# Performance work log

Measured on AMD Instinct MI355X. Metric: run time of the kernel, lower is better.

## Reference

```python
import jax, jax.numpy as jnp
import numpy as np

B, IN_DIM, HIDDEN, N_CLASSES, D_Z = 16384, 1024, 2048, 8, 256
LN_EPS = 1e-5  # torch.nn.LayerNorm default


def _l2_normalize(x, axis=1, eps=1e-12):
    # matches F.normalize: x / max(||x||, eps)
    n = jnp.sqrt(jnp.sum(x * x, axis=axis, keepdims=True))
    return x / jnp.maximum(n, eps)


def setup_inputs() -> dict:
    key = jax.random.key(0)
    ks = jax.random.split(key, 9)
    s1 = 1.0 / np.sqrt(IN_DIM)
    s2 = 1.0 / np.sqrt(HIDDEN)
    return {
        "feat": jax.random.normal(ks[0], (B, IN_DIM), dtype=jnp.float32),
        "z_cat": jax.random.normal(ks[1], (B, D_Z), dtype=jnp.float32),
        "mu_cat": jax.random.normal(ks[2], (N_CLASSES, D_Z), dtype=jnp.float32),
        "ln_gamma": jnp.ones((N_CLASSES, IN_DIM), dtype=jnp.float32),
        "ln_beta": jnp.zeros((N_CLASSES, IN_DIM), dtype=jnp.float32),
        "W1": jax.random.uniform(ks[3], (N_CLASSES, IN_DIM, HIDDEN), jnp.float32, -s1, s1),
        "b1": jax.random.uniform(ks[4], (N_CLASSES, HIDDEN), jnp.float32, -s1, s1),
        "W2": jax.random.uniform(ks[5], (N_CLASSES, HIDDEN, N_CLASSES), jnp.float32, -s2, s2),
        "b2": jax.random.uniform(ks[6], (N_CLASSES, N_CLASSES), jnp.float32, -s2, s2),
        "tau_gate": 1,
    }


def reference(feat, z_cat, mu_cat, ln_gamma, ln_beta, W1, b1, W2, b2, tau_gate):
    # --- cosine-similarity softmax gate ---
    zn = _l2_normalize(z_cat, axis=1)            # [B, Dz]
    mun = _l2_normalize(mu_cat, axis=1)          # [E, Dz]
    sims = zn @ mun.T                            # [B, E]
    tau = max(1e-6, float(tau_gate))
    w = jax.nn.softmax(sims / tau, axis=1)       # [B, E]

    # --- batched experts: LN -> Linear -> ReLU -> (Dropout=identity, eval) -> Linear ---
    mu = jnp.mean(feat, axis=-1, keepdims=True)
    var = jnp.mean(jnp.square(feat - mu), axis=-1, keepdims=True)
    xhat = (feat - mu) * jax.lax.rsqrt(var + LN_EPS)            # [B, D] (shared)
    x_e = xhat[None] * ln_gamma[:, None, :] + ln_beta[:, None, :]  # [E, B, D]
    h = jax.nn.relu(jnp.einsum('ebd,edh->ebh', x_e, W1) + b1[:, None, :])  # [E, B, H]
    exp_logits = jnp.einsum('ebh,ehc->ebc', h, W2) + b2[:, None, :]        # [E, B, C]

    # --- gate-weighted sum over experts ---
    logits = jnp.einsum('ebc,be->bc', exp_logits, w)  # [B, C]
    return logits, w
```

## Files before the change

kernel.cpp:

```cpp
#include <hip/hip_runtime.h>
#include <hip/hip_bf16.h>
#include <cstdint>

#define NB     16384
#define DIN    1024
#define HID    2048
#define NE     8
#define NC     8
#define DZ     256

#define BK2    64
#define NKT    (DIN / BK2)
#define GRID_MAIN 256

typedef short bf16x8 __attribute__((ext_vector_type(8)));
typedef float f32x4  __attribute__((ext_vector_type(4)));

__device__ __forceinline__ unsigned short f2bf(float f) {
    unsigned int u = __float_as_uint(f);
    unsigned int r = (u + 0x7FFFu + ((u >> 16) & 1u)) >> 16;
    return (unsigned short)r;
}

__device__ __forceinline__ void async_copy16(const void* g, void* l) {
    __builtin_amdgcn_global_load_lds(
        (const __attribute__((address_space(1))) unsigned int*)g,
        (__attribute__((address_space(3))) unsigned int*)l, 16, 0, 0);
}

__global__ __launch_bounds__(256) void k_pre(const float* __restrict__ feat,
                                             unsigned short* __restrict__ xhat,
                                             const float* __restrict__ z,
                                             const float* __restrict__ mu,
                                             const int* __restrict__ tau_i,
                                             const float* __restrict__ b2,
                                             float* __restrict__ wout,
                                             float* __restrict__ logits) {
    if (blockIdx.x < NB) {
        int row = blockIdx.x;
        int t = threadIdx.x;
        float4 v = *(const float4*)&feat[(size_t)row * DIN + t * 4];
        float s  = v.x + v.y + v.z + v.w;
        float sq = v.x * v.x + v.y * v.y + v.z * v.z + v.w * v.w;
#pragma unroll
        for (int off = 32; off; off >>= 1) {
            s  += __shfl_down(s, off);
            sq += __shfl_down(sq, off);
        }
        __shared__ float ls[8];
        int w = t >> 6, l = t & 63;
        if (l == 0) { ls[w] = s; ls[4 + w] = sq; }
        __syncthreads();
        s  = ls[0] + ls[1] + ls[2] + ls[3];
        sq = ls[4] + ls[5] + ls[6] + ls[7];
        float mean = s * (1.f / DIN);
        float var  = sq * (1.f / DIN) - mean * mean;
        float r = 1.0f / sqrtf(var + 1e-5f);
        uint2 p;
        p.x = (unsigned)f2bf((v.x - mean) * r) | ((unsigned)f2bf((v.y - mean) * r) << 16);
        p.y = (unsigned)f2bf((v.z - mean) * r) | ((unsigned)f2bf((v.w - mean) * r) << 16);
        *(uint2*)&xhat[(size_t)row * DIN + t * 4] = p;
    } else {
        int row = (blockIdx.x - NB) * 4 + (threadIdx.x >> 6);
        int l = threadIdx.x & 63;
        float4 zv = *(const float4*)&z[(size_t)row * DZ + l * 4];
        float zz = zv.x * zv.x + zv.y * zv.y + zv.z * zv.z + zv.w * zv.w;
        float dots[NE], mm[NE];
#pragma unroll
        for (int e = 0; e < NE; ++e) {
            float4 m = *(const float4*)&mu[e * DZ + l * 4];
            dots[e] = zv.x * m.x + zv.y * m.y + zv.z * m.z + zv.w * m.w;
            mm[e]   = m.x * m.x + m.y * m.y + m.z * m.z + m.w * m.w;
        }
#pragma unroll
        for (int off = 32; off; off >>= 1) {
            zz += __shfl_xor(zz, off);
#pragma unroll
            for (int e = 0; e < NE; ++e) {
                dots[e] += __shfl_xor(dots[e], off);
                mm[e]   += __shfl_xor(mm[e], off);
            }
        }
        float zn = fmaxf(sqrtf(zz), 1e-12f);
        float tau = fmaxf(1e-6f, (float)tau_i[0]);
        float s[NE], mx = -1e30f;
#pragma unroll
        for (int e = 0; e < NE; ++e) {
            s[e] = dots[e] / (zn * fmaxf(sqrtf(mm[e]), 1e-12f)) / tau;
            mx = fmaxf(mx, s[e]);
        }
        float sum = 0.f;
#pragma unroll
        for (int e = 0; e < NE; ++e) { s[e] = expf(s[e] - mx); sum += s[e]; }
        float inv = 1.f / sum;
        if (l < NE) {
            wout[(size_t)row * NE + l] = s[l] * inv;
            float acc = 0.f;
#pragma unroll
            for (int e = 0; e < NE; ++e) acc += s[e] * inv * b2[e * NC + l];
            logits[(size_t)row * NC + l] = acc;
        }
    }
}

__global__ __launch_bounds__(256) void k_w2prep(const float* __restrict__ W2,
                                                const float* __restrict__ b1,
                                                unsigned short* __restrict__ w2t,
                                                float* __restrict__ b1p) {
    int i = blockIdx.x * 256 + threadIdx.x;
    int e = i >> 15;
    int rem = i & 32767;
    int c = rem >> 11;
    int h = rem & 2047;
    float v = (c < NC) ? W2[((size_t)(e * HID + h)) * NC + c] : 0.f;
    w2t[i] = f2bf(v);
    if (i < NE * HID) b1p[i] = b1[i];
}

__global__ __launch_bounds__(256) void k_w1prep(const float* __restrict__ W1,
                                                const float* __restrict__ gamma,
                                                const float* __restrict__ beta,
                                                unsigned short* __restrict__ w1t,
                                                float* __restrict__ b1p) {
    __shared__ float tile[64][65];
    int e  = blockIdx.z;
    int d0 = blockIdx.y * 64;
    int h0 = blockIdx.x * 64;
    int tx = threadIdx.x & 15, ty = threadIdx.x >> 4;
#pragma unroll
    for (int rr = 0; rr < 4; ++rr) {
        int d = ty + rr * 16;
        float4 v = *(const float4*)&W1[((size_t)e * DIN + d0 + d) * HID + h0 + tx * 4];
        tile[tx * 4 + 0][d] = v.x;
        tile[tx * 4 + 1][d] = v.y;
        tile[tx * 4 + 2][d] = v.z;
        tile[tx * 4 + 3][d] = v.w;
    }
    __syncthreads();
    float4 g = *(const float4*)&gamma[(size_t)e * DIN + d0 + tx * 4];
#pragma unroll
    for (int rr = 0; rr < 4; ++rr) {
        int h = ty + rr * 16;
        uint2 p;
        p.x = (unsigned)f2bf(tile[h][tx * 4 + 0] * g.x) |
              ((unsigned)f2bf(tile[h][tx * 4 + 1] * g.y) << 16);
        p.y = (unsigned)f2bf(tile[h][tx * 4 + 2] * g.z) |
              ((unsigned)f2bf(tile[h][tx * 4 + 3] * g.w) << 16);
        *(uint2*)&w1t[((size_t)e * HID + h0 + h) * DIN + d0 + tx * 4] = p;
    }
    if (threadIdx.x < 64) {
        int h = threadIdx.x;
        float sacc = 0.f;
        for (int r = 0; r < 64; ++r)
            sacc += beta[(size_t)e * DIN + d0 + r] * tile[h][r];
        atomicAdd(&b1p[(size_t)e * HID + h0 + h], sacc);
    }
}


#define WAITV(n_) asm volatile("s_waitcnt vmcnt(" #n_ ")" ::: "memory")
#define BAR()  do { __builtin_amdgcn_s_barrier(); __builtin_amdgcn_sched_barrier(0); } while (0)

#define STAGE(gAp_, gBp_, kt64_, par_) do {                                   \
    char* da_ = (char*)lds + ((par_) << 16) + (t << 4);                       \
    const size_t ko_ = sbase + (size_t)(kt64_) * BK2;                         \
    async_copy16((gAp_) + ko_,          da_);                                 \
    async_copy16((gAp_) + ko_ + 65536,  da_ + 8192);                          \
    async_copy16((gAp_) + ko_ + 131072, da_ + 16384);                         \
    async_copy16((gAp_) + ko_ + 196608, da_ + 24576);                         \
    async_copy16((gBp_) + ko_,          da_ + 32768);                         \
    async_copy16((gBp_) + ko_ + 65536,  da_ + 40960);                         \
    async_copy16((gBp_) + ko_ + 131072, da_ + 49152);                         \
    async_copy16((gBp_) + ko_ + 196608, da_ + 57344);                         \
} while (0)

#define KBODY(par_) do {                                                      \
    const short* la_ = (const short*)(lds + ((par_) << 16));                  \
    const short* lb_ = la_ + 16384;                                           \
    {                                                                         \
        bf16x8 bF_[4];                                                        \
        _Pragma("unroll")                                                     \
        for (int j_ = 0; j_ < 4; ++j_)                                        \
            bF_[j_] = *(const bf16x8*)&lb_[(wn + 16 * j_ + ml) * BK2 + csw0]; \
        __builtin_amdgcn_s_setprio(1);                                        \
        _Pragma("unroll")                                                     \
        for (int i_ = 0; i_ < 8; ++i_) {                                      \
            const bf16x8 aF_ =                                                \
                *(const bf16x8*)&la_[(wm + 16 * i_ + ml) * BK2 + csw0];       \
            _Pragma("unroll")                                                 \
            for (int j_ = 0; j_ < 4; ++j_)                                    \
                acc[i_][j_] = __builtin_amdgcn_mfma_f32_16x16x32_bf16(        \
                    aF_, bF_[j_], acc[i_][j_], 0, 0, 0);                      \
        }                                                                     \
        __builtin_amdgcn_s_setprio(0);                                        \
    }                                                                         \
    {                                                                         \
        const int cs1_ = csw0 ^ 32;                                           \
        bf16x8 bF_[4];                                                        \
        _Pragma("unroll")                                                     \
        for (int j_ = 0; j_ < 4; ++j_)                                        \
            bF_[j_] = *(const bf16x8*)&lb_[(wn + 16 * j_ + ml) * BK2 + cs1_]; \
        __builtin_amdgcn_s_setprio(1);                                        \
        _Pragma("unroll")                                                     \
        for (int i_ = 0; i_ < 8; ++i_) {                                      \
            const bf16x8 aF_ =                                                \
                *(const bf16x8*)&la_[(wm + 16 * i_ + ml) * BK2 + cs1_];       \
            _Pragma("unroll")                                                 \
            for (int j_ = 0; j_ < 4; ++j_)                                    \
                acc[i_][j_] = __builtin_amdgcn_mfma_f32_16x16x32_bf16(        \
                    aF_, bF_[j_], acc[i_][j_], 0, 0, 0);                      \
        }                                                                     \
        __builtin_amdgcn_s_setprio(0);                                        \
    }                                                                         \
} while (0)

__global__ __launch_bounds__(512, 2) void moe_main(
        const unsigned short* __restrict__ xhat,
        const unsigned short* __restrict__ w1t,
        const float* __restrict__ b1p,
        const unsigned short* __restrict__ w2t,
        const float* __restrict__ wg,
        float* __restrict__ logits) {
    __shared__ __align__(16) char lds[131072];

    const int t  = threadIdx.x;
    const int w  = t >> 6, l = t & 63;
    const int q  = l >> 4, ml = l & 15;
    const int wm = (w >> 2) * 128;
    const int wn = (w & 3) * 64;
    const int csw0 = (q ^ (ml & 7)) * 8;
    const size_t sbase = (size_t)(t >> 3) * DIN +
                         (size_t)(((t & 7) ^ ((t >> 3) & 7)) * 8);

    const int e    = blockIdx.x & 7;
    const int slot = blockIdx.x >> 3;
    char* myht = (char*)lds + 65536 + w * 5120;
    const unsigned short* eA = w1t + (size_t)e * HID * DIN;

    STAGE(eA, xhat + (size_t)slot * 256 * DIN, 0, 0);

    for (int pr = 0; pr < 2; ++pr) {
        const int b0 = (pr * 32 + slot) * 256;
        const unsigned short* gB = xhat + (size_t)b0 * DIN;

        f32x4 acc2[4];
#pragma unroll
        for (int tb = 0; tb < 4; ++tb) acc2[tb] = (f32x4){0.f, 0.f, 0.f, 0.f};

        for (int ms = 0; ms < 8; ++ms) {
            const int hid0 = ms * 256;
            const unsigned short* gA = eA + (size_t)hid0 * DIN;

            f32x4 acc[8][4];
#pragma unroll
            for (int i = 0; i < 8; ++i)
#pragma unroll
                for (int j = 0; j < 4; ++j) acc[i][j] = (f32x4){0.f, 0.f, 0.f, 0.f};

#pragma unroll 1
            for (int kt = 0; kt < NKT - 1; ++kt) {
                WAITV(0);
                BAR();
                STAGE(gA, gB, kt + 1, (kt + 1) & 1);
                KBODY(kt & 1);
            }
            WAITV(0);
            BAR();
            if (!(pr == 1 && ms == 7)) {
                const unsigned short* gAn = (ms == 7) ? eA : gA + (size_t)256 * DIN;
                const unsigned short* gBn = (ms == 7) ? gB + (size_t)8192 * DIN : gB;
                STAGE(gAn, gBn, 0, 0);
            }
            KBODY(1);
            BAR();

#pragma unroll
            for (int s = 0; s < 4; ++s) {
#pragma unroll
                for (int i2 = 0; i2 < 2; ++i2) {
                    const int i = 2 * s + i2;
                    const float4 bias = *(const float4*)
                        &b1p[(size_t)e * HID + hid0 + wm + 16 * i + 4 * q];
#pragma unroll
                    for (int j = 0; j < 4; ++j) {
                        float v0 = fmaxf(acc[i][j].x + bias.x, 0.f);
                        float v1 = fmaxf(acc[i][j].y + bias.y, 0.f);
                        float v2 = fmaxf(acc[i][j].z + bias.z, 0.f);
                        float v3 = fmaxf(acc[i][j].w + bias.w, 0.f);
                        uint2 p;
                        p.x = (unsigned)f2bf(v0) | ((unsigned)f2bf(v1) << 16);
                        p.y = (unsigned)f2bf(v2) | ((unsigned)f2bf(v3) << 16);
                        *(uint2*)(myht + (16 * j + ml) * 80 + (16 * i2 + 4 * q) * 2) = p;
                    }
                }
                const bf16x8 b2f = *(const bf16x8*)&w2t[((size_t)e * 16 + ml) * HID +
                                                        hid0 + wm + 32 * s + 8 * q];
#pragma unroll
                for (int tb = 0; tb < 4; ++tb) {
                    const bf16x8 a2f =
                        *(const bf16x8*)(myht + (16 * tb + ml) * 80 + q * 16);
                    acc2[tb] = __builtin_amdgcn_mfma_f32_16x16x32_bf16(
                        a2f, b2f, acc2[tb], 0, 0, 0);
                }
            }
        }

        __syncthreads();
        float* red = (float*)(lds + 106496);
        if (w >= 4) {
            float* dst = red + ((w & 3) * 64 + l) * 16;
#pragma unroll
            for (int tb = 0; tb < 4; ++tb)
#pragma unroll
                for (int r = 0; r < 4; ++r) dst[tb * 4 + r] = acc2[tb][r];
        }
        __syncthreads();
        if (w < 4) {
            const float* src = red + (w * 64 + l) * 16;
            if (ml < NC) {
#pragma unroll
                for (int tb = 0; tb < 4; ++tb) {
#pragma unroll
                    for (int r = 0; r < 4; ++r) {
                        float v = acc2[tb][r] + src[tb * 4 + r];
                        const int bg = b0 + wn + 16 * tb + 4 * q + r;
                        atomicAdd(&logits[(size_t)bg * NC + ml],
                                  wg[(size_t)bg * NE + e] * v);
                    }
                }
            }
        }
    }
}

extern "C" void kernel_launch(void* const* d_in, const int* in_sizes, int n_in,
                              void* d_out, int out_size, void* d_ws, size_t ws_size,
                              hipStream_t stream) {
    const float* feat  = (const float*)d_in[0];
    const float* z     = (const float*)d_in[1];
    const float* mu    = (const float*)d_in[2];
    const float* gamma = (const float*)d_in[3];
    const float* beta  = (const float*)d_in[4];
    const float* W1    = (const float*)d_in[5];
    const float* b1    = (const float*)d_in[6];
    const float* W2    = (const float*)d_in[7];
    const float* b2    = (const float*)d_in[8];
    const int*   tau   = (const int*)d_in[9];

    float* logits = (float*)d_out;
    float* wout   = logits + (size_t)NB * NC;

    char* ws = (char*)d_ws;
    unsigned short* xhat = (unsigned short*)ws;
    unsigned short* w1t  = (unsigned short*)(ws + 33554432);
    unsigned short* w2t  = (unsigned short*)(ws + 67108864);
    float*          b1p  = (float*)(ws + 67633152);

    k_pre<<<NB + NB / 4, 256, 0, stream>>>(feat, xhat, z, mu, tau, b2, wout, logits);
    k_w2prep<<<(NE * 16 * HID) / 256, 256, 0, stream>>>(W2, b1, w2t, b1p);
    k_w1prep<<<dim3(HID / 64, DIN / 64, NE), 256, 0, stream>>>(W1, gamma, beta, w1t, b1p);
    moe_main<<<dim3(GRID_MAIN), 512, 0, stream>>>(xhat, w1t, b1p, w2t, wout, logits);
}
```

Baseline: 692.3 us.

## Triple-buffer W1 tiles in LDS and load xhat fragments directly into registers

The GEMM1 main loop now stages only the W1 (A) tiles through LDS in a three-deep ring, with vmcnt waits that keep two loads in flight. The xhat (B) fragments are loaded straight from global memory into two register sets that alternate between k-steps. This halves LDS traffic and async copies per step and deepens prefetch, aiming to hide global latency better. In exchange it uses more LDS (152KB, which may limit occupancy to one block per CU) and more VGPRs for the register double buffer, and the B loads are less coalesced.

```diff
diff --git a/kernel.cpp b/kernel.cpp
--- a/kernel.cpp
+++ b/kernel.cpp
@@ -161,57 +161,44 @@
 #define WAITV(n_) asm volatile("s_waitcnt vmcnt(" #n_ ")" ::: "memory")
 #define BAR()  do { __builtin_amdgcn_s_barrier(); __builtin_amdgcn_sched_barrier(0); } while (0)
 
-#define STAGE(gAp_, gBp_, kt64_, par_) do {                                   \
-    char* da_ = (char*)lds + ((par_) << 16) + (t << 4);                       \
-    const size_t ko_ = sbase + (size_t)(kt64_) * BK2;                         \
+#define ISSA(gAp_, kt_, bIdx_) do {                                           \
+    char* da_ = (char*)lds + (bIdx_) * 32768 + (t << 4);                      \
+    const size_t ko_ = sbase + (size_t)(kt_) * BK2;                           \
     async_copy16((gAp_) + ko_,          da_);                                 \
     async_copy16((gAp_) + ko_ + 65536,  da_ + 8192);                          \
     async_copy16((gAp_) + ko_ + 131072, da_ + 16384);                         \
     async_copy16((gAp_) + ko_ + 196608, da_ + 24576);                         \
-    async_copy16((gBp_) + ko_,          da_ + 32768);                         \
-    async_copy16((gBp_) + ko_ + 65536,  da_ + 40960);                         \
-    async_copy16((gBp_) + ko_ + 131072, da_ + 49152);                         \
-    async_copy16((gBp_) + ko_ + 196608, da_ + 57344);                         \
 } while (0)
 
-#define KBODY(par_) do {                                                      \
-    const short* la_ = (const short*)(lds + ((par_) << 16));                  \
-    const short* lb_ = la_ + 16384;                                           \
-    {                                                                         \
-        bf16x8 bF_[4];                                                        \
+#define ISSB(SET_, gBp_, kt_) do {                                            \
+    const size_t kb_ = (size_t)(kt_) * BK2;                                   \
+    _Pragma("unroll")                                                         \
+    for (int j_ = 0; j_ < 4; ++j_) {                                          \
+        SET_[j_]     = *(const bf16x8*)&(gBp_)[bOff[j_] + kb_];               \
+        SET_[4 + j_] = *(const bf16x8*)&(gBp_)[bOff[j_] + kb_ + 32];          \
+    }                                                                         \
+} while (0)
+
+#define COMP(base_, SET_) do {                                                \
+    const short* la_ = (const short*)(base_);                                 \
+    __builtin_amdgcn_s_setprio(1);                                            \
+    _Pragma("unroll")                                                         \
+    for (int i_ = 0; i_ < 8; ++i_) {                                          \
+        const bf16x8 aF_ = *(const bf16x8*)&la_[(wm + 16 * i_ + ml) * 64 + csw0]; \
         _Pragma("unroll")                                                     \
         for (int j_ = 0; j_ < 4; ++j_)                                        \
-            bF_[j_] = *(const bf16x8*)&lb_[(wn + 16 * j_ + ml) * BK2 + csw0]; \
-        __builtin_amdgcn_s_setprio(1);                                        \
-        _Pragma("unroll")                                                     \
-        for (int i_ = 0; i_ < 8; ++i_) {                                      \
-            const bf16x8 aF_ =                                                \
-                *(const bf16x8*)&la_[(wm + 16 * i_ + ml) * BK2 + csw0];       \
-            _Pragma("unroll")                                                 \
-            for (int j_ = 0; j_ < 4; ++j_)                                    \
-                acc[i_][j_] = __builtin_amdgcn_mfma_f32_16x16x32_bf16(        \
-                    aF_, bF_[j_], acc[i_][j_], 0, 0, 0);                      \
-        }                                                                     \
-        __builtin_amdgcn_s_setprio(0);                                        \
+            acc[i_][j_] = __builtin_amdgcn_mfma_f32_16x16x32_bf16(            \
+                aF_, SET_[j_], acc[i_][j_], 0, 0, 0);                         \
     }                                                                         \
-    {                                                                         \
-        const int cs1_ = csw0 ^ 32;                                           \
-        bf16x8 bF_[4];                                                        \
+    _Pragma("unroll")                                                         \
+    for (int i_ = 0; i_ < 8; ++i_) {                                          \
+        const bf16x8 aF_ = *(const bf16x8*)&la_[(wm + 16 * i_ + ml) * 64 + (csw0 ^ 32)]; \
         _Pragma("unroll")                                                     \
         for (int j_ = 0; j_ < 4; ++j_)                                        \
-            bF_[j_] = *(const bf16x8*)&lb_[(wn + 16 * j_ + ml) * BK2 + cs1_]; \
-        __builtin_amdgcn_s_setprio(1);                                        \
-        _Pragma("unroll")                                                     \
-        for (int i_ = 0; i_ < 8; ++i_) {                                      \
-            const bf16x8 aF_ =                                                \
-                *(const bf16x8*)&la_[(wm + 16 * i_ + ml) * BK2 + cs1_];       \
-            _Pragma("unroll")                                                 \
-            for (int j_ = 0; j_ < 4; ++j_)                                    \
-                acc[i_][j_] = __builtin_amdgcn_mfma_f32_16x16x32_bf16(        \
-                    aF_, bF_[j_], acc[i_][j_], 0, 0, 0);                      \
-        }                                                                     \
-        __builtin_amdgcn_s_setprio(0);                                        \
+            acc[i_][j_] = __builtin_amdgcn_mfma_f32_16x16x32_bf16(            \
+                aF_, SET_[4 + j_], acc[i_][j_], 0, 0, 0);                     \
     }                                                                         \
+    __builtin_amdgcn_s_setprio(0);                                            \
 } while (0)
 
 __global__ __launch_bounds__(512, 2) void moe_main(
@@ -221,7 +208,7 @@
         const unsigned short* __restrict__ w2t,
         const float* __restrict__ wg,
         float* __restrict__ logits) {
-    __shared__ __align__(16) char lds[131072];
+    __shared__ __align__(16) char lds[155648];
 
     const int t  = threadIdx.x;
     const int w  = t >> 6, l = t & 63;
@@ -234,10 +221,22 @@
 
     const int e    = blockIdx.x & 7;
     const int slot = blockIdx.x >> 3;
-    char* myht = (char*)lds + 65536 + w * 5120;
+    char* myht = (char*)lds + 98304 + w * 5120;
     const unsigned short* eA = w1t + (size_t)e * HID * DIN;
 
-    STAGE(eA, xhat + (size_t)slot * 256 * DIN, 0, 0);
+    size_t bOff[4];
+#pragma unroll
+    for (int j = 0; j < 4; ++j)
+        bOff[j] = (size_t)(wn + 16 * j + ml) * DIN + q * 8;
+
+    bf16x8 B0[8], B1[8];
+    int bcur = 0;
+
+    {
+        const unsigned short* gB0 = xhat + (size_t)(slot * 256) * DIN;
+        ISSA(eA, 0, 0); ISSB(B0, gB0, 0);
+        ISSA(eA, 1, 1); ISSB(B1, gB0, 1);
+    }
 
     for (int pr = 0; pr < 2; ++pr) {
         const int b0 = (pr * 32 + slot) * 256;
@@ -250,6 +249,10 @@
         for (int ms = 0; ms < 8; ++ms) {
             const int hid0 = ms * 256;
             const unsigned short* gA = eA + (size_t)hid0 * DIN;
+            const bool last = (pr == 1) && (ms == 7);
+            const unsigned short* gAn = (ms == 7) ? eA : gA + (size_t)256 * DIN;
+            const unsigned short* gBn = (ms == 7)
+                ? xhat + (size_t)(((pr + 1) * 32 + slot) * 256) * DIN : gB;
 
             f32x4 acc[8][4];
 #pragma unroll
@@ -258,21 +261,32 @@
                 for (int j = 0; j < 4; ++j) acc[i][j] = (f32x4){0.f, 0.f, 0.f, 0.f};
 
 #pragma unroll 1
-            for (int kt = 0; kt < NKT - 1; ++kt) {
-                WAITV(0);
+            for (int kp = 0; kp < 8; ++kp) {
+                WAITV(12);
                 BAR();
-                STAGE(gA, gB, kt + 1, (kt + 1) & 1);
-                KBODY(kt & 1);
+                {
+                    int bi = bcur + 2; if (bi >= 3) bi -= 3;
+                    if (kp < 7)      ISSA(gA, 2 * kp + 2, bi);
+                    else if (!last)  ISSA(gAn, 0, bi);
+                }
+                COMP((char*)lds + bcur * 32768, B0);
+                if (kp < 7)      ISSB(B0, gB, 2 * kp + 2);
+                else if (!last)  ISSB(B0, gBn, 0);
+                bcur = (bcur == 2) ? 0 : bcur + 1;
+
+                if (kp == 7) { WAITV(0); }
+                else         { WAITV(12); }
+                BAR();
+                {
+                    int bi = bcur + 2; if (bi >= 3) bi -= 3;
+                    if (kp < 7)      ISSA(gA, 2 * kp + 3, bi);
+                    else if (!last)  ISSA(gAn, 1, bi);
+                }
+                COMP((char*)lds + bcur * 32768, B1);
+                if (kp < 7)      ISSB(B1, gB, 2 * kp + 3);
+                else if (!last)  ISSB(B1, gBn, 1);
+                bcur = (bcur == 2) ? 0 : bcur + 1;
             }
-            WAITV(0);
-            BAR();
-            if (!(pr == 1 && ms == 7)) {
-                const unsigned short* gAn = (ms == 7) ? eA : gA + (size_t)256 * DIN;
-                const unsigned short* gBn = (ms == 7) ? gB + (size_t)8192 * DIN : gB;
-                STAGE(gAn, gBn, 0, 0);
-            }
-            KBODY(1);
-            BAR();
 
 #pragma unroll
             for (int s = 0; s < 4; ++s) {
@@ -306,7 +320,7 @@
         }
 
         __syncthreads();
-        float* red = (float*)(lds + 106496);
+        float* red = (float*)(lds + 139264);
         if (w >= 4) {
             float* dst = red + ((w & 3) * 64 + l) * 16;
 #pragma unroll
```

New measurement: 1.771 ms. 2.56x slower.
